# Kernel optimization log

Hardware: AMD Instinct MI355X
Metric: run time of the kernel (lower is better)

Reference implementation:

```python
import jax, jax.numpy as jnp
import numpy as np

PROJ_DIM = 8192
INPUT_DIM = 512
THRESH = 1e-08


def _signed_sqrt(x):
    return jnp.sign(x) * jnp.sqrt(jnp.abs(x))


def _make_sketch_matrix(key, input_dim, proj_dim):
    kh, ks = jax.random.split(key)
    h = jax.random.randint(kh, (input_dim,), 0, proj_dim)
    s = jnp.sign(jax.random.uniform(ks, (input_dim,), minval=-1.0, maxval=1.0)).astype(jnp.float32)
    M = jnp.zeros((input_dim, proj_dim), dtype=jnp.float32)
    return M.at[jnp.arange(input_dim), h].set(s)


def setup_inputs() -> dict:
    key = jax.random.key(0)
    kx, k1, k2 = jax.random.split(key, 3)
    x = jax.random.normal(kx, (32, 14, 14, INPUT_DIM), dtype=jnp.float32)
    M1 = _make_sketch_matrix(k1, INPUT_DIM, PROJ_DIM)
    M2 = _make_sketch_matrix(k2, INPUT_DIM, PROJ_DIM)
    return {"x": x, "M1": M1, "M2": M2}


def reference(x, M1, M2):
    B, H, W, C = x.shape
    x_flat = x.reshape(-1, C)                      # [B*H*W, C]
    # count-sketch projections (dense matmul, as in the original layer)
    p1 = (x_flat @ M1).astype(jnp.complex64)       # [B*H*W, P]
    p2 = (x_flat @ M2).astype(jnp.complex64)
    # circular convolution via FFT
    sketch = jnp.fft.fft(p1, axis=-1) * jnp.fft.fft(p2, axis=-1)
    y = jnp.real(jnp.fft.ifft(sketch, axis=-1)).astype(jnp.float32)
    y = y.reshape(B, H, W, -1).sum(axis=(1, 2))    # sum-pool over spatial dims -> [B, P]
    y = _signed_sqrt(y)
    # tf.nn.l2_normalize(x, axis=1, epsilon=1e-10)
    inv_norm = jax.lax.rsqrt(jnp.maximum(jnp.sum(y * y, axis=1, keepdims=True), 1e-10))
    return y * inv_norm
```

## Files before the change

kernel.cpp:

```cpp
#include <hip/hip_runtime.h>
#include <math.h>

#define PROJ 8192
#define CDIM 512
#define HWPOS 196
#define NBATCH 32
#define NSLAB 7
#define NUNITF 8
#define NPAGES 8

typedef __attribute__((ext_vector_type(8))) short   short8;
typedef __attribute__((ext_vector_type(4))) float   f32x4;

__device__ __forceinline__ unsigned short f2bf(float f) {
    unsigned u = __float_as_uint(f);
    u += 0x7fff + ((u >> 16) & 1);
    return (unsigned short)(u >> 16);
}
__device__ __forceinline__ float bf2f(unsigned short h) {
    return __uint_as_float(((unsigned)h) << 16);
}

__device__ __forceinline__ void lds_fadd(float* p, float v) {
    __attribute__((address_space(3))) float* lp =
        (__attribute__((address_space(3))) float*)p;
    asm volatile("ds_add_f32 %0, %1" : : "v"(lp), "v"(v) : "memory");
}

__global__ __launch_bounds__(256) void extract_kernel(
    const float* __restrict__ M1, const float* __restrict__ M2,
    int* __restrict__ h1, float* __restrict__ s1,
    int* __restrict__ h2, float* __restrict__ s2,
    float* __restrict__ norm)
{
    const int row = blockIdx.x;
    const float* M = blockIdx.y ? M2 : M1;
    int*   h = blockIdx.y ? h2 : h1;
    float* s = blockIdx.y ? s2 : s1;
    const float* mrow = M + (size_t)row * PROJ;

    if (blockIdx.x == 0 && blockIdx.y == 0 && threadIdx.x < NBATCH)
        norm[threadIdx.x] = 0.0f;

    for (int i = threadIdx.x * 4; i < PROJ; i += 256 * 4) {
        float4 v = *(const float4*)(mrow + i);
        if (v.x != 0.0f) { h[row] = i + 0; s[row] = v.x; }
        if (v.y != 0.0f) { h[row] = i + 1; s[row] = v.y; }
        if (v.z != 0.0f) { h[row] = i + 2; s[row] = v.z; }
        if (v.w != 0.0f) { h[row] = i + 3; s[row] = v.w; }
    }
}

__global__ __launch_bounds__(256) void prep_kernel(
    const float* __restrict__ x,
    unsigned short* __restrict__ XThi, unsigned short* __restrict__ XTlo)
{
    const int ks  = blockIdx.x;
    const int bat = blockIdx.y;
    const int tid = threadIdx.x;
    __shared__ float xt[32][513];

    const float* xb = x + (size_t)bat * HWPOS * CDIM;
    const int k0 = ks * 32;
#pragma unroll
    for (int i = 0; i < 16; ++i) {
        const int idx = i * 1024 + tid * 4;
        const int kr  = idx >> 9;
        const int c   = idx & 511;
        float4 v = make_float4(0.f, 0.f, 0.f, 0.f);
        if (k0 + kr < HWPOS) v = *(const float4*)(xb + (size_t)(k0 + kr) * CDIM + c);
        xt[kr][c+0] = v.x; xt[kr][c+1] = v.y; xt[kr][c+2] = v.z; xt[kr][c+3] = v.w;
    }
    __syncthreads();

    unsigned short* ohi = XThi + ((size_t)bat * NSLAB + ks) * 16384;
    unsigned short* olo = XTlo + ((size_t)bat * NSLAB + ks) * 16384;
#pragma unroll
    for (int i = 0; i < 8; ++i) {
        const int ch   = i * 256 + tid;
        const int c16  = ch & 15;
        const int quad = (ch >> 4) & 3;
        const int cgrp = ch >> 6;
        const int c    = cgrp * 16 + c16;
        short8 vh, vl;
#pragma unroll
        for (int j = 0; j < 8; ++j) {
            float f = xt[quad * 8 + j][c];
            unsigned short h = f2bf(f);
            vh[j] = (short)h;
            vl[j] = (short)f2bf(f - bf2f(h));
        }
        *(short8*)(ohi + ch * 8) = vh;
        *(short8*)(olo + ch * 8) = vl;
    }
}

__global__ __launch_bounds__(256) void gramscatter_kernel(
    const unsigned short* __restrict__ XThi, const unsigned short* __restrict__ XTlo,
    const int* __restrict__ h1, const float* __restrict__ s1,
    const int* __restrict__ h2, const float* __restrict__ s2,
    float* __restrict__ pbins)
{
    const int id  = blockIdx.x;
    const int sub = id >> 3;
    const int u   = sub & 7;
    const int bat = (id & 7) + 8 * (sub >> 3);
    const bool pair  = (u < 2);
    const bool doMir = (u >= 2);
    const int  k6    = u - 2;

    const int tid  = threadIdx.x;
    const int w    = tid >> 6;
    const int lane = tid & 63;
    const int rowq = w >> 1, colq = w & 1;

    __shared__ __align__(16) unsigned short Sbuf[2][4][4096];
    __shared__ float bins[PROJ];
    __shared__ int   th1[256]; __shared__ float ts1[256];
    __shared__ int   th2[256]; __shared__ float ts2[256];

    for (int i = tid; i < PROJ; i += 256) bins[i] = 0.f;

    for (int rep = 0; rep < 2; ++rep) {
        if (rep == 1 && !pair) break;
        const int bi = pair ? (2 * u + rep) : (int)((0x211000u >> (k6 * 4)) & 15);
        const int bj = pair ? (2 * u + rep) : (int)((0x332321u >> (k6 * 4)) & 15);

        {
            const int g = (tid < 128) ? (bi * 128 + tid) : (bj * 128 + tid - 128);
            th1[tid] = h1[g]; ts1[tid] = s1[g];
            th2[tid] = h2[g]; ts2[tid] = s2[g];
        }

        const int tile = (w < 2) ? bi : bj;
        const unsigned short* srcbase = ((w & 1) ? XTlo : XThi)
                                      + (size_t)bat * NSLAB * 16384 + (size_t)tile * 4096;

        {
            const unsigned short* src = srcbase;
            unsigned short* dst = &Sbuf[0][w][0];
#pragma unroll
            for (int i = 0; i < 8; ++i)
                __builtin_amdgcn_global_load_lds(
                    (const __attribute__((address_space(1))) void*)(src + i * 512 + lane * 8),
                    (__attribute__((address_space(3))) void*)(dst + i * 512), 16, 0, 0);
        }

        f32x4 acc[16];
#pragma unroll
        for (int i = 0; i < 16; ++i) { acc[i][0]=0.f; acc[i][1]=0.f; acc[i][2]=0.f; acc[i][3]=0.f; }

        for (int ks = 0; ks < NSLAB; ++ks) {
            __syncthreads();
            const int buf = ks & 1;

            if (ks + 1 < NSLAB) {
                const unsigned short* src = srcbase + (size_t)(ks + 1) * 16384;
                unsigned short* dst = &Sbuf[buf ^ 1][w][0];
#pragma unroll
                for (int i = 0; i < 8; ++i)
                    __builtin_amdgcn_global_load_lds(
                        (const __attribute__((address_space(1))) void*)(src + i * 512 + lane * 8),
                        (__attribute__((address_space(3))) void*)(dst + i * 512), 16, 0, 0);
            }

            short8 ah[4], al[4], bh[4], bl[4];
#pragma unroll
            for (int t = 0; t < 4; ++t) {
                ah[t] = *(const short8*)&Sbuf[buf][0][(rowq * 4 + t) * 512 + lane * 8];
                al[t] = *(const short8*)&Sbuf[buf][1][(rowq * 4 + t) * 512 + lane * 8];
                bh[t] = *(const short8*)&Sbuf[buf][2][(colq * 4 + t) * 512 + lane * 8];
                bl[t] = *(const short8*)&Sbuf[buf][3][(colq * 4 + t) * 512 + lane * 8];
            }
#pragma unroll
            for (int mt = 0; mt < 4; ++mt)
#pragma unroll
                for (int nt = 0; nt < 4; ++nt) {
                    const int idx = mt * 4 + nt;
                    acc[idx] = __builtin_amdgcn_mfma_f32_16x16x32_bf16(ah[mt], bh[nt], acc[idx], 0, 0, 0);
                    acc[idx] = __builtin_amdgcn_mfma_f32_16x16x32_bf16(ah[mt], bl[nt], acc[idx], 0, 0, 0);
                    acc[idx] = __builtin_amdgcn_mfma_f32_16x16x32_bf16(al[mt], bh[nt], acc[idx], 0, 0, 0);
                }
        }

        int   h2c[4], h1c[4];
        float s2c[4], s1c[4];
#pragma unroll
        for (int nt = 0; nt < 4; ++nt) {
            const int cl = colq * 64 + nt * 16 + (lane & 15);
            h2c[nt] = th2[128 + cl]; s2c[nt] = ts2[128 + cl];
            h1c[nt] = th1[128 + cl]; s1c[nt] = ts1[128 + cl];
        }
        const int quad = lane >> 4;
#pragma unroll
        for (int mt = 0; mt < 4; ++mt)
#pragma unroll
            for (int reg = 0; reg < 4; ++reg) {
                const int rl = rowq * 64 + mt * 16 + quad * 4 + reg;
                const int   h1r = th1[rl]; const float s1r = ts1[rl];
                const int   h2r = th2[rl]; const float s2r = ts2[rl];
#pragma unroll
                for (int nt = 0; nt < 4; ++nt) {
                    const float v = acc[mt * 4 + nt][reg];
                    lds_fadd(&bins[(h1r + h2c[nt]) & (PROJ - 1)], s1r * s2c[nt] * v);
                    if (doMir)
                        lds_fadd(&bins[(h1c[nt] + h2r) & (PROJ - 1)], s1c[nt] * s2r * v);
                }
            }
        __syncthreads();
    }

    float* dst = pbins + ((size_t)bat * NPAGES + u) * PROJ;
    for (int i = tid * 4; i < PROJ; i += 1024)
        *(float4*)(dst + i) = *(const float4*)&bins[i];
}

__global__ __launch_bounds__(512) void finalize_kernel(
    const float* __restrict__ pbins, float* __restrict__ out)
{
    const int bat = blockIdx.x;
    const int tid = threadIdx.x;
    const float* pb = pbins + (size_t)bat * NPAGES * PROJ;

    float4 y0, y1, y2, y3;
    float local = 0.f;

#pragma unroll
    for (int c = 0; c < 4; ++c) {
        const int base = c * 2048 + tid * 4;
        float4 a = make_float4(0.f, 0.f, 0.f, 0.f);
#pragma unroll
        for (int t = 0; t < NPAGES; ++t) {
            float4 p = *(const float4*)(pb + (size_t)t * PROJ + base);
            a.x += p.x; a.y += p.y; a.z += p.z; a.w += p.w;
        }
        local += fabsf(a.x) + fabsf(a.y) + fabsf(a.z) + fabsf(a.w);
        float4 sv;
        sv.x = (a.x >= 0.f) ? sqrtf(a.x) : -sqrtf(-a.x);
        sv.y = (a.y >= 0.f) ? sqrtf(a.y) : -sqrtf(-a.y);
        sv.z = (a.z >= 0.f) ? sqrtf(a.z) : -sqrtf(-a.z);
        sv.w = (a.w >= 0.f) ? sqrtf(a.w) : -sqrtf(-a.w);
        if (c == 0) y0 = sv; else if (c == 1) y1 = sv; else if (c == 2) y2 = sv; else y3 = sv;
    }

#pragma unroll
    for (int off = 32; off > 0; off >>= 1) local += __shfl_down(local, off, 64);

    __shared__ float wred[8];
    __shared__ float sinv;
    if ((tid & 63) == 0) wred[tid >> 6] = local;
    __syncthreads();
    if (tid == 0) {
        float t = 0.f;
#pragma unroll
        for (int i = 0; i < 8; ++i) t += wred[i];
        sinv = rsqrtf(fmaxf(t, 1e-10f));
    }
    __syncthreads();
    const float inv = sinv;

    float* ob = out + (size_t)bat * PROJ;
#pragma unroll
    for (int c = 0; c < 4; ++c) {
        float4 sv = (c == 0) ? y0 : (c == 1) ? y1 : (c == 2) ? y2 : y3;
        sv.x *= inv; sv.y *= inv; sv.z *= inv; sv.w *= inv;
        *(float4*)(ob + c * 2048 + tid * 4) = sv;
    }
}

extern "C" void kernel_launch(void* const* d_in, const int* in_sizes, int n_in,
                              void* d_out, int out_size, void* d_ws, size_t ws_size,
                              hipStream_t stream)
{
    const float* x  = (const float*)d_in[0];
    const float* M1 = (const float*)d_in[1];
    const float* M2 = (const float*)d_in[2];
    float* out = (float*)d_out;

    char* ws = (char*)d_ws;
    int*            h1    = (int*)   (ws + 0);
    float*          s1    = (float*) (ws + 2048);
    int*            h2    = (int*)   (ws + 4096);
    float*          s2    = (float*) (ws + 6144);
    float*          norm  = (float*) (ws + 8192);
    unsigned short* XThi  = (unsigned short*)(ws + 16384);
    unsigned short* XTlo  = (unsigned short*)(ws + 7356416);
    float*          pbins = (float*) (ws + 14696448);

    extract_kernel<<<dim3(512, 2), 256, 0, stream>>>(M1, M2, h1, s1, h2, s2, norm);
    prep_kernel<<<dim3(NSLAB, NBATCH), 256, 0, stream>>>(x, XThi, XTlo);
    gramscatter_kernel<<<NUNITF * NBATCH, 256, 0, stream>>>(XThi, XTlo, h1, s1, h2, s2, pbins);
    finalize_kernel<<<NBATCH, 512, 0, stream>>>(pbins, out);
}
```

Measured before the change: 161.2 us.

## Replace LDS atomic scatter with precomputed CSR gather of Gram tiles

Removes the LDS float atomic scatter of Gram tile entries into bins. Instead it precomputes a per-tile-pair CSR (histogram, scan, place kernels) that maps each output bin to signed Gram entries, and each block gathers its bins from the tile staged in LDS. Mirrored tiles become separate segments (16 per batch instead of 8 units with mirror duplication), so the grid doubles and more pages must be reduced in finalize. It adds three small kernels and a data-dependent inner loop in exchange for atomic-free accumulation, and folds the x prep into the same launch as the histogram.

New measurement: 203.4 us. 1.26x slower.

```diff
diff --git a/kernel.cpp b/kernel.cpp
--- a/kernel.cpp
+++ b/kernel.cpp
@@ -6,8 +6,7 @@
 #define HWPOS 196
 #define NBATCH 32
 #define NSLAB 7
-#define NUNITF 8
-#define NPAGES 8
+#define NSEG 16
 
 typedef __attribute__((ext_vector_type(8))) short   short8;
 typedef __attribute__((ext_vector_type(4))) float   f32x4;
@@ -21,26 +20,34 @@
     return __uint_as_float(((unsigned)h) << 16);
 }
 
-__device__ __forceinline__ void lds_fadd(float* p, float v) {
-    __attribute__((address_space(3))) float* lp =
-        (__attribute__((address_space(3))) float*)p;
-    asm volatile("ds_add_f32 %0, %1" : : "v"(lp), "v"(v) : "memory");
+#define BI_PACK 0x2110002110003210ULL
+#define BJ_PACK 0x3323213323213210ULL
+
+__device__ __forceinline__ void seg_entry(int seg, int e,
+    const int* __restrict__ h1, const float* __restrict__ s1,
+    const int* __restrict__ h2, const float* __restrict__ s2,
+    int& bin, int& sg)
+{
+    const int bi = (int)((BI_PACK >> (seg * 4)) & 15);
+    const int bj = (int)((BJ_PACK >> (seg * 4)) & 15);
+    const int r = e >> 7, c = e & 127;
+    int gi, gj;
+    if (seg < 10) { gi = bi * 128 + r; gj = bj * 128 + c; }
+    else          { gi = bj * 128 + c; gj = bi * 128 + r; }
+    bin = (h1[gi] + h2[gj]) & (PROJ - 1);
+    sg  = (int)((__float_as_uint(s1[gi]) ^ __float_as_uint(s2[gj])) >> 31);
 }
 
 __global__ __launch_bounds__(256) void extract_kernel(
     const float* __restrict__ M1, const float* __restrict__ M2,
     int* __restrict__ h1, float* __restrict__ s1,
-    int* __restrict__ h2, float* __restrict__ s2,
-    float* __restrict__ norm)
+    int* __restrict__ h2, float* __restrict__ s2)
 {
     const int row = blockIdx.x;
     const float* M = blockIdx.y ? M2 : M1;
     int*   h = blockIdx.y ? h2 : h1;
     float* s = blockIdx.y ? s2 : s1;
     const float* mrow = M + (size_t)row * PROJ;
-
-    if (blockIdx.x == 0 && blockIdx.y == 0 && threadIdx.x < NBATCH)
-        norm[threadIdx.x] = 0.0f;
 
     for (int i = threadIdx.x * 4; i < PROJ; i += 256 * 4) {
         float4 v = *(const float4*)(mrow + i);
@@ -51,63 +58,150 @@
     }
 }
 
-__global__ __launch_bounds__(256) void prep_kernel(
+__global__ __launch_bounds__(256) void combo_kernel(
     const float* __restrict__ x,
-    unsigned short* __restrict__ XThi, unsigned short* __restrict__ XTlo)
-{
-    const int ks  = blockIdx.x;
-    const int bat = blockIdx.y;
-    const int tid = threadIdx.x;
-    __shared__ float xt[32][513];
-
-    const float* xb = x + (size_t)bat * HWPOS * CDIM;
-    const int k0 = ks * 32;
-#pragma unroll
-    for (int i = 0; i < 16; ++i) {
-        const int idx = i * 1024 + tid * 4;
-        const int kr  = idx >> 9;
-        const int c   = idx & 511;
-        float4 v = make_float4(0.f, 0.f, 0.f, 0.f);
-        if (k0 + kr < HWPOS) v = *(const float4*)(xb + (size_t)(k0 + kr) * CDIM + c);
-        xt[kr][c+0] = v.x; xt[kr][c+1] = v.y; xt[kr][c+2] = v.z; xt[kr][c+3] = v.w;
-    }
-    __syncthreads();
-
-    unsigned short* ohi = XThi + ((size_t)bat * NSLAB + ks) * 16384;
-    unsigned short* olo = XTlo + ((size_t)bat * NSLAB + ks) * 16384;
-#pragma unroll
-    for (int i = 0; i < 8; ++i) {
-        const int ch   = i * 256 + tid;
-        const int c16  = ch & 15;
-        const int quad = (ch >> 4) & 3;
-        const int cgrp = ch >> 6;
-        const int c    = cgrp * 16 + c16;
-        short8 vh, vl;
-#pragma unroll
-        for (int j = 0; j < 8; ++j) {
-            float f = xt[quad * 8 + j][c];
-            unsigned short h = f2bf(f);
-            vh[j] = (short)h;
-            vl[j] = (short)f2bf(f - bf2f(h));
-        }
-        *(short8*)(ohi + ch * 8) = vh;
-        *(short8*)(olo + ch * 8) = vl;
-    }
-}
-
-__global__ __launch_bounds__(256) void gramscatter_kernel(
-    const unsigned short* __restrict__ XThi, const unsigned short* __restrict__ XTlo,
+    unsigned short* __restrict__ XThi, unsigned short* __restrict__ XTlo,
     const int* __restrict__ h1, const float* __restrict__ s1,
     const int* __restrict__ h2, const float* __restrict__ s2,
+    unsigned* __restrict__ bh)
+{
+    __shared__ __align__(16) char smem[32 * 513 * 4];
+    const int tid = threadIdx.x;
+
+    if (blockIdx.x < 224) {
+        float (*xt)[513] = (float(*)[513])smem;
+        const int bat = blockIdx.x >> 3;
+        const int ks  = blockIdx.x % NSLAB;
+        const int bt  = blockIdx.x / NSLAB;
+        (void)bat;
+        const float* xb = x + (size_t)bt * HWPOS * CDIM;
+        const int k0 = ks * 32;
+#pragma unroll
+        for (int i = 0; i < 16; ++i) {
+            const int idx = i * 1024 + tid * 4;
+            const int kr  = idx >> 9;
+            const int c   = idx & 511;
+            float4 v = make_float4(0.f, 0.f, 0.f, 0.f);
+            if (k0 + kr < HWPOS) v = *(const float4*)(xb + (size_t)(k0 + kr) * CDIM + c);
+            xt[kr][c+0] = v.x; xt[kr][c+1] = v.y; xt[kr][c+2] = v.z; xt[kr][c+3] = v.w;
+        }
+        __syncthreads();
+
+        unsigned short* ohi = XThi + ((size_t)bt * NSLAB + ks) * 16384;
+        unsigned short* olo = XTlo + ((size_t)bt * NSLAB + ks) * 16384;
+#pragma unroll
+        for (int i = 0; i < 8; ++i) {
+            const int ch   = i * 256 + tid;
+            const int c16  = ch & 15;
+            const int quad = (ch >> 4) & 3;
+            const int cgrp = ch >> 6;
+            const int c    = cgrp * 16 + c16;
+            short8 vh, vl;
+#pragma unroll
+            for (int j = 0; j < 8; ++j) {
+                float f = xt[quad * 8 + j][c];
+                unsigned short h = f2bf(f);
+                vh[j] = (short)h;
+                vl[j] = (short)f2bf(f - bf2f(h));
+            }
+            *(short8*)(ohi + ch * 8) = vh;
+            *(short8*)(olo + ch * 8) = vl;
+        }
+    } else {
+        unsigned* lh = (unsigned*)smem;
+        const int blk = blockIdx.x - 224;
+        const int seg = blk >> 2, q = blk & 3;
+        for (int i = tid; i < PROJ; i += 256) lh[i] = 0u;
+        __syncthreads();
+#pragma unroll
+        for (int k = 0; k < 16; ++k) {
+            const int e = q * 4096 + k * 256 + tid;
+            int bin, sg;
+            seg_entry(seg, e, h1, s1, h2, s2, bin, sg);
+            atomicAdd(&lh[bin], 1u);
+        }
+        __syncthreads();
+        unsigned* dst = bh + (size_t)blk * PROJ;
+        for (int i = tid; i < PROJ; i += 256) dst[i] = lh[i];
+    }
+}
+
+__global__ __launch_bounds__(256) void scan_kernel(
+    unsigned* __restrict__ bh, unsigned* __restrict__ binbase)
+{
+    const int seg = blockIdx.x;
+    const int tid = threadIdx.x;
+    __shared__ unsigned sc[256];
+    __shared__ unsigned carry;
+    if (tid == 0) carry = 0u;
+    __syncthreads();
+
+    unsigned* b0 = bh + (size_t)(seg * 4 + 0) * PROJ;
+    unsigned* b1 = bh + (size_t)(seg * 4 + 1) * PROJ;
+    unsigned* b2 = bh + (size_t)(seg * 4 + 2) * PROJ;
+    unsigned* b3 = bh + (size_t)(seg * 4 + 3) * PROJ;
+
+    for (int k = 0; k < 32; ++k) {
+        const int b = k * 256 + tid;
+        const unsigned q0 = b0[b], q1 = b1[b], q2 = b2[b], q3 = b3[b];
+        const unsigned tot = q0 + q1 + q2 + q3;
+        sc[tid] = tot;
+        __syncthreads();
+        for (int off = 1; off < 256; off <<= 1) {
+            unsigned t = (tid >= off) ? sc[tid - off] : 0u;
+            __syncthreads();
+            sc[tid] += t;
+            __syncthreads();
+        }
+        const unsigned rc   = carry;
+        const unsigned incl = sc[tid];
+        const unsigned base = rc + incl - tot;
+        binbase[(size_t)seg * 8193 + b] = base;
+        b0[b] = base;
+        b1[b] = base + q0;
+        b2[b] = base + q0 + q1;
+        b3[b] = base + q0 + q1 + q2;
+        __syncthreads();
+        if (tid == 255) carry = rc + incl;
+        __syncthreads();
+    }
+    if (tid == 0) binbase[(size_t)seg * 8193 + 8192] = carry;
+}
+
+__global__ __launch_bounds__(256) void place_kernel(
+    const int* __restrict__ h1, const float* __restrict__ s1,
+    const int* __restrict__ h2, const float* __restrict__ s2,
+    const unsigned* __restrict__ bh, unsigned short* __restrict__ csr)
+{
+    const int blk = blockIdx.x;
+    const int seg = blk >> 2, q = blk & 3;
+    const int tid = threadIdx.x;
+    __shared__ unsigned lr[PROJ];
+    for (int i = tid; i < PROJ; i += 256) lr[i] = 0u;
+    __syncthreads();
+    const unsigned* mybase = bh + (size_t)blk * PROJ;
+    unsigned short* cs = csr + (size_t)seg * 16384;
+#pragma unroll
+    for (int k = 0; k < 16; ++k) {
+        const int e = q * 4096 + k * 256 + tid;
+        int bin, sg;
+        seg_entry(seg, e, h1, s1, h2, s2, bin, sg);
+        const unsigned rk = atomicAdd(&lr[bin], 1u);
+        cs[mybase[bin] + rk] = (unsigned short)(e | (sg << 15));
+    }
+}
+
+__global__ __launch_bounds__(256) void gramgather_kernel(
+    const unsigned short* __restrict__ XThi, const unsigned short* __restrict__ XTlo,
+    const unsigned* __restrict__ binbase, const unsigned short* __restrict__ csr,
     float* __restrict__ pbins)
 {
     const int id  = blockIdx.x;
     const int sub = id >> 3;
-    const int u   = sub & 7;
-    const int bat = (id & 7) + 8 * (sub >> 3);
-    const bool pair  = (u < 2);
-    const bool doMir = (u >= 2);
-    const int  k6    = u - 2;
+    const int tp  = sub & 15;
+    const int bat = (id & 7) + 8 * (sub >> 4);
+    const int bi = (int)((BI_PACK >> (tp * 4)) & 15);
+    const int bj = (int)((BJ_PACK >> (tp * 4)) & 15);
 
     const int tid  = threadIdx.x;
     const int w    = tid >> 6;
@@ -115,30 +209,32 @@
     const int rowq = w >> 1, colq = w & 1;
 
     __shared__ __align__(16) unsigned short Sbuf[2][4][4096];
-    __shared__ float bins[PROJ];
-    __shared__ int   th1[256]; __shared__ float ts1[256];
-    __shared__ int   th2[256]; __shared__ float ts2[256];
-
-    for (int i = tid; i < PROJ; i += 256) bins[i] = 0.f;
-
-    for (int rep = 0; rep < 2; ++rep) {
-        if (rep == 1 && !pair) break;
-        const int bi = pair ? (2 * u + rep) : (int)((0x211000u >> (k6 * 4)) & 15);
-        const int bj = pair ? (2 * u + rep) : (int)((0x332321u >> (k6 * 4)) & 15);
-
-        {
-            const int g = (tid < 128) ? (bi * 128 + tid) : (bj * 128 + tid - 128);
-            th1[tid] = h1[g]; ts1[tid] = s1[g];
-            th2[tid] = h2[g]; ts2[tid] = s2[g];
-        }
-
-        const int tile = (w < 2) ? bi : bj;
-        const unsigned short* srcbase = ((w & 1) ? XTlo : XThi)
-                                      + (size_t)bat * NSLAB * 16384 + (size_t)tile * 4096;
-
-        {
-            const unsigned short* src = srcbase;
-            unsigned short* dst = &Sbuf[0][w][0];
+
+    const int tile = (w < 2) ? bi : bj;
+    const unsigned short* srcbase = ((w & 1) ? XTlo : XThi)
+                                  + (size_t)bat * NSLAB * 16384 + (size_t)tile * 4096;
+
+    {
+        const unsigned short* src = srcbase;
+        unsigned short* dst = &Sbuf[0][w][0];
+#pragma unroll
+        for (int i = 0; i < 8; ++i)
+            __builtin_amdgcn_global_load_lds(
+                (const __attribute__((address_space(1))) void*)(src + i * 512 + lane * 8),
+                (__attribute__((address_space(3))) void*)(dst + i * 512), 16, 0, 0);
+    }
+
+    f32x4 acc[16];
+#pragma unroll
+    for (int i = 0; i < 16; ++i) { acc[i][0]=0.f; acc[i][1]=0.f; acc[i][2]=0.f; acc[i][3]=0.f; }
+
+    for (int ks = 0; ks < NSLAB; ++ks) {
+        __syncthreads();
+        const int buf = ks & 1;
+
+        if (ks + 1 < NSLAB) {
+            const unsigned short* src = srcbase + (size_t)(ks + 1) * 16384;
+            unsigned short* dst = &Sbuf[buf ^ 1][w][0];
 #pragma unroll
             for (int i = 0; i < 8; ++i)
                 __builtin_amdgcn_global_load_lds(
@@ -146,73 +242,56 @@
                     (__attribute__((address_space(3))) void*)(dst + i * 512), 16, 0, 0);
         }
 
-        f32x4 acc[16];
-#pragma unroll
-        for (int i = 0; i < 16; ++i) { acc[i][0]=0.f; acc[i][1]=0.f; acc[i][2]=0.f; acc[i][3]=0.f; }
-
-        for (int ks = 0; ks < NSLAB; ++ks) {
-            __syncthreads();
-            const int buf = ks & 1;
-
-            if (ks + 1 < NSLAB) {
-                const unsigned short* src = srcbase + (size_t)(ks + 1) * 16384;
-                unsigned short* dst = &Sbuf[buf ^ 1][w][0];
-#pragma unroll
-                for (int i = 0; i < 8; ++i)
-                    __builtin_amdgcn_global_load_lds(
-                        (const __attribute__((address_space(1))) void*)(src + i * 512 + lane * 8),
-                        (__attribute__((address_space(3))) void*)(dst + i * 512), 16, 0, 0);
+        short8 ah[4], al[4], bh4[4], bl[4];
+#pragma unroll
+        for (int t = 0; t < 4; ++t) {
+            ah[t]  = *(const short8*)&Sbuf[buf][0][(rowq * 4 + t) * 512 + lane * 8];
+            al[t]  = *(const short8*)&Sbuf[buf][1][(rowq * 4 + t) * 512 + lane * 8];
+            bh4[t] = *(const short8*)&Sbuf[buf][2][(colq * 4 + t) * 512 + lane * 8];
+            bl[t]  = *(const short8*)&Sbuf[buf][3][(colq * 4 + t) * 512 + lane * 8];
+        }
+#pragma unroll
+        for (int mt = 0; mt < 4; ++mt)
+#pragma unroll
+            for (int nt = 0; nt < 4; ++nt) {
+                const int idx = mt * 4 + nt;
+                acc[idx] = __builtin_amdgcn_mfma_f32_16x16x32_bf16(ah[mt], bh4[nt], acc[idx], 0, 0, 0);
+                acc[idx] = __builtin_amdgcn_mfma_f32_16x16x32_bf16(ah[mt], bl[nt],  acc[idx], 0, 0, 0);
+                acc[idx] = __builtin_amdgcn_mfma_f32_16x16x32_bf16(al[mt], bh4[nt], acc[idx], 0, 0, 0);
             }
-
-            short8 ah[4], al[4], bh[4], bl[4];
-#pragma unroll
-            for (int t = 0; t < 4; ++t) {
-                ah[t] = *(const short8*)&Sbuf[buf][0][(rowq * 4 + t) * 512 + lane * 8];
-                al[t] = *(const short8*)&Sbuf[buf][1][(rowq * 4 + t) * 512 + lane * 8];
-                bh[t] = *(const short8*)&Sbuf[buf][2][(colq * 4 + t) * 512 + lane * 8];
-                bl[t] = *(const short8*)&Sbuf[buf][3][(colq * 4 + t) * 512 + lane * 8];
+    }
+
+    __syncthreads();
+    float* tileL = (float*)Sbuf;
+    const int quad = lane >> 4;
+#pragma unroll
+    for (int mt = 0; mt < 4; ++mt)
+#pragma unroll
+        for (int reg = 0; reg < 4; ++reg) {
+            const int rl = rowq * 64 + mt * 16 + quad * 4 + reg;
+#pragma unroll
+            for (int nt = 0; nt < 4; ++nt) {
+                const int cl = colq * 64 + nt * 16 + (lane & 15);
+                tileL[rl * 128 + cl] = acc[mt * 4 + nt][reg];
             }
-#pragma unroll
-            for (int mt = 0; mt < 4; ++mt)
-#pragma unroll
-                for (int nt = 0; nt < 4; ++nt) {
-                    const int idx = mt * 4 + nt;
-                    acc[idx] = __builtin_amdgcn_mfma_f32_16x16x32_bf16(ah[mt], bh[nt], acc[idx], 0, 0, 0);
-                    acc[idx] = __builtin_amdgcn_mfma_f32_16x16x32_bf16(ah[mt], bl[nt], acc[idx], 0, 0, 0);
-                    acc[idx] = __builtin_amdgcn_mfma_f32_16x16x32_bf16(al[mt], bh[nt], acc[idx], 0, 0, 0);
-                }
-        }
-
-        int   h2c[4], h1c[4];
-        float s2c[4], s1c[4];
-#pragma unroll
-        for (int nt = 0; nt < 4; ++nt) {
-            const int cl = colq * 64 + nt * 16 + (lane & 15);
-            h2c[nt] = th2[128 + cl]; s2c[nt] = ts2[128 + cl];
-            h1c[nt] = th1[128 + cl]; s1c[nt] = ts1[128 + cl];
-        }
-        const int quad = lane >> 4;
-#pragma unroll
-        for (int mt = 0; mt < 4; ++mt)
-#pragma unroll
-            for (int reg = 0; reg < 4; ++reg) {
-                const int rl = rowq * 64 + mt * 16 + quad * 4 + reg;
-                const int   h1r = th1[rl]; const float s1r = ts1[rl];
-                const int   h2r = th2[rl]; const float s2r = ts2[rl];
-#pragma unroll
-                for (int nt = 0; nt < 4; ++nt) {
-                    const float v = acc[mt * 4 + nt][reg];
-                    lds_fadd(&bins[(h1r + h2c[nt]) & (PROJ - 1)], s1r * s2c[nt] * v);
-                    if (doMir)
-                        lds_fadd(&bins[(h1c[nt] + h2r) & (PROJ - 1)], s1c[nt] * s2r * v);
-                }
-            }
-        __syncthreads();
-    }
-
-    float* dst = pbins + ((size_t)bat * NPAGES + u) * PROJ;
-    for (int i = tid * 4; i < PROJ; i += 1024)
-        *(float4*)(dst + i) = *(const float4*)&bins[i];
+        }
+    __syncthreads();
+
+    const unsigned* bb = binbase + (size_t)tp * 8193;
+    const unsigned short* cs = csr + (size_t)tp * 16384;
+    float* page = pbins + ((size_t)bat * NSEG + tp) * PROJ;
+#pragma unroll 4
+    for (int k = 0; k < 32; ++k) {
+        const int b = k * 256 + tid;
+        const unsigned s0 = bb[b], e0 = bb[b + 1];
+        float a = 0.f;
+        for (unsigned p = s0; p < e0; ++p) {
+            const unsigned ent = cs[p];
+            const float tv = tileL[ent & 0x3FFF];
+            a += (ent & 0x8000) ? -tv : tv;
+        }
+        page[b] = a;
+    }
 }
 
 __global__ __launch_bounds__(512) void finalize_kernel(
@@ -220,7 +299,7 @@
 {
     const int bat = blockIdx.x;
     const int tid = threadIdx.x;
-    const float* pb = pbins + (size_t)bat * NPAGES * PROJ;
+    const float* pb = pbins + (size_t)bat * NSEG * PROJ;
 
     float4 y0, y1, y2, y3;
     float local = 0.f;
@@ -230,7 +309,7 @@
         const int base = c * 2048 + tid * 4;
         float4 a = make_float4(0.f, 0.f, 0.f, 0.f);
 #pragma unroll
-        for (int t = 0; t < NPAGES; ++t) {
+        for (int t = 0; t < NSEG; ++t) {
             float4 p = *(const float4*)(pb + (size_t)t * PROJ + base);
             a.x += p.x; a.y += p.y; a.z += p.z; a.w += p.w;
         }
@@ -278,17 +357,21 @@
     float* out = (float*)d_out;
 
     char* ws = (char*)d_ws;
-    int*            h1    = (int*)   (ws + 0);
-    float*          s1    = (float*) (ws + 2048);
-    int*            h2    = (int*)   (ws + 4096);
-    float*          s2    = (float*) (ws + 6144);
-    float*          norm  = (float*) (ws + 8192);
-    unsigned short* XThi  = (unsigned short*)(ws + 16384);
-    unsigned short* XTlo  = (unsigned short*)(ws + 7356416);
-    float*          pbins = (float*) (ws + 14696448);
-
-    extract_kernel<<<dim3(512, 2), 256, 0, stream>>>(M1, M2, h1, s1, h2, s2, norm);
-    prep_kernel<<<dim3(NSLAB, NBATCH), 256, 0, stream>>>(x, XThi, XTlo);
-    gramscatter_kernel<<<NUNITF * NBATCH, 256, 0, stream>>>(XThi, XTlo, h1, s1, h2, s2, pbins);
+    int*            h1      = (int*)   (ws + 0);
+    float*          s1      = (float*) (ws + 2048);
+    int*            h2      = (int*)   (ws + 4096);
+    float*          s2      = (float*) (ws + 6144);
+    unsigned*       binbase = (unsigned*)(ws + 16384);
+    unsigned short* csr     = (unsigned short*)(ws + 540736);
+    unsigned short* XThi    = (unsigned short*)(ws + 1065984);
+    unsigned short* XTlo    = (unsigned short*)(ws + 8406016);
+    float*          pbins   = (float*) (ws + 15746048);
+    unsigned*       bh      = (unsigned*)pbins;
+
+    extract_kernel<<<dim3(512, 2), 256, 0, stream>>>(M1, M2, h1, s1, h2, s2);
+    combo_kernel<<<288, 256, 0, stream>>>(x, XThi, XTlo, h1, s1, h2, s2, bh);
+    scan_kernel<<<NSEG, 256, 0, stream>>>(bh, binbase);
+    place_kernel<<<64, 256, 0, stream>>>(h1, s1, h2, s2, bh, csr);
+    gramgather_kernel<<<NSEG * NBATCH, 256, 0, stream>>>(XThi, XTlo, binbase, csr, pbins);
     finalize_kernel<<<NBATCH, 512, 0, stream>>>(pbins, out);
 }
```
